# Kernel tuning notes

Measured on AMD Instinct MI355X. Metric: run time of the kernel, lower is better.

The kernel has to match this reference:

```python
import jax, jax.numpy as jnp
import numpy as np

N, E = 50000, 800000
NFEAT, HID, NHEAD, NCLASS = 256, 32, 8, 40
NEG_SLOPE = 0.2


def gat_conv(x, src, dst, W, a_src, a_dst, bias, heads, out_ch, concat):
    n = x.shape[0]
    h = (x @ W).reshape(n, heads, out_ch)              # [N, H, C]
    alpha_src = jnp.einsum('nhc,hc->nh', h, a_src)     # [N, H]
    alpha_dst = jnp.einsum('nhc,hc->nh', h, a_dst)
    e = jax.nn.leaky_relu(alpha_src[src] + alpha_dst[dst], NEG_SLOPE)  # [E, H]
    # segment softmax over incoming edges of each dst node
    m = jax.ops.segment_max(e, dst, num_segments=n)
    ex = jnp.exp(e - m[dst])
    s = jax.ops.segment_sum(ex, dst, num_segments=n)
    alpha = ex / (s[dst] + 1e-16)                      # [E, H]
    out = jax.ops.segment_sum(h[src] * alpha[:, :, None], dst, num_segments=n)  # [N, H, C]
    out = out.reshape(n, heads * out_ch) if concat else out.mean(axis=1)
    return out + bias


def setup_inputs() -> dict:
    key = jax.random.key(0)
    ks = jax.random.split(key, 12)
    x = jax.random.normal(ks[0], (N, NFEAT), dtype=jnp.float32)
    edge_index = jax.random.randint(ks[1], (2, E), 0, N, dtype=jnp.int64)
    edge_attr = jax.random.normal(ks[2], (E, 8), dtype=jnp.float32)  # unused by the model
    s1 = 1.0 / np.sqrt(NFEAT)
    s2 = 1.0 / np.sqrt(HID * NHEAD)
    W1 = jax.random.normal(ks[3], (NFEAT, NHEAD * HID), dtype=jnp.float32) * s1
    att_src1 = jax.random.normal(ks[4], (NHEAD, HID), dtype=jnp.float32) * 0.1
    att_dst1 = jax.random.normal(ks[5], (NHEAD, HID), dtype=jnp.float32) * 0.1
    b1 = jnp.zeros((NHEAD * HID,), dtype=jnp.float32)
    W2 = jax.random.normal(ks[6], (NHEAD * HID, NCLASS), dtype=jnp.float32) * s2
    att_src2 = jax.random.normal(ks[7], (1, NCLASS), dtype=jnp.float32) * 0.1
    att_dst2 = jax.random.normal(ks[8], (1, NCLASS), dtype=jnp.float32) * 0.1
    b2 = jnp.zeros((NCLASS,), dtype=jnp.float32)
    return {"x": x, "edge_index": edge_index, "edge_attr": edge_attr,
            "W1": W1, "att_src1": att_src1, "att_dst1": att_dst1, "b1": b1,
            "W2": W2, "att_src2": att_src2, "att_dst2": att_dst2, "b2": b2}


def reference(x, edge_index, edge_attr, W1, att_src1, att_dst1, b1, W2, att_src2, att_dst2, b2):
    # eval mode: dropout is identity. GATConv adds self-loops by default.
    n = x.shape[0]
    loops = jnp.arange(n, dtype=edge_index.dtype)
    src = jnp.concatenate([edge_index[0], loops])
    dst = jnp.concatenate([edge_index[1], loops])
    h = jax.nn.elu(gat_conv(x, src, dst, W1, att_src1, att_dst1, b1, NHEAD, HID, True))
    final = gat_conv(h, src, dst, W2, att_src2, att_dst2, b2, 1, NCLASS, False)
    return final, jax.nn.log_softmax(final, axis=1)
```

## Files before the change

kernel.cpp:

```cpp
#include <hip/hip_runtime.h>
#include <hip/hip_bf16.h>
#include <hip/hip_fp16.h>
#include <math.h>

#define NN 50000
#define EE 800000
#define ET 850000
#define F1 256
#define NHEAD 8
#define HID 32
#define NCLASS 40
#define NEG 0.2f

typedef __attribute__((ext_vector_type(8))) _Float16 half8_t;
typedef __attribute__((ext_vector_type(4))) float float4_t;

__device__ __forceinline__ int clampN(int v) {
    return v < 0 ? 0 : (v >= NN ? NN - 1 : v);
}
__device__ __forceinline__ unsigned short f2h(float f) {
    __half h = __float2half(f);
    return __builtin_bit_cast(unsigned short, h);
}
__device__ __forceinline__ float h2f(unsigned short u) {
    __half h = __builtin_bit_cast(__half, u);
    return __half2float(h);
}
__device__ __forceinline__ float hlo2f(unsigned int u) {
    return h2f((unsigned short)(u & 0xFFFFu));
}
__device__ __forceinline__ float hhi2f(unsigned int u) {
    return h2f((unsigned short)(u >> 16));
}

__global__ __launch_bounds__(256) void hist_kernel(const int* __restrict__ ei, int* __restrict__ deg,
                                                   unsigned int* __restrict__ pack) {
    int t = blockIdx.x * 256 + threadIdx.x;
    if (t >= ET) return;
    int d = (t < EE) ? ei[EE + t] : (t - EE);
    d = clampN(d);
    int r = atomicAdd(&deg[d], 1);
    pack[t] = ((unsigned)d << 15) | (unsigned)r;
}

__global__ __launch_bounds__(256) void scan1_kernel(const int* __restrict__ deg, int* __restrict__ off, int* __restrict__ bsum) {
    __shared__ int lds[256];
    int b = blockIdx.x, tid = threadIdx.x;
    int base = b * 1024 + tid * 4;
    int v0 = (base + 0 < NN) ? deg[base + 0] : 0;
    int v1 = (base + 1 < NN) ? deg[base + 1] : 0;
    int v2 = (base + 2 < NN) ? deg[base + 2] : 0;
    int v3 = (base + 3 < NN) ? deg[base + 3] : 0;
    int s1 = v0 + v1, s2 = s1 + v2, s3 = s2 + v3;
    lds[tid] = s3;
    __syncthreads();
    for (int o = 1; o < 256; o <<= 1) {
        int t = (tid >= o) ? lds[tid - o] : 0;
        __syncthreads();
        if (tid >= o) lds[tid] += t;
        __syncthreads();
    }
    int excl = tid ? lds[tid - 1] : 0;
    if (base + 0 < NN) off[base + 1] = excl + v0;
    if (base + 1 < NN) off[base + 2] = excl + s1;
    if (base + 2 < NN) off[base + 3] = excl + s2;
    if (base + 3 < NN) off[base + 4] = excl + s3;
    if (tid == 255) bsum[b] = lds[255];
}

__global__ __launch_bounds__(256) void scan2_kernel(int* __restrict__ bsum, int nb) {
    __shared__ int lds[256];
    int tid = threadIdx.x;
    lds[tid] = (tid < nb) ? bsum[tid] : 0;
    __syncthreads();
    for (int o = 1; o < 256; o <<= 1) {
        int t = (tid >= o) ? lds[tid - o] : 0;
        __syncthreads();
        if (tid >= o) lds[tid] += t;
        __syncthreads();
    }
    if (tid < nb) bsum[tid] = lds[tid];
}

__global__ __launch_bounds__(256) void scan3_kernel(int* __restrict__ off, const int* __restrict__ bsum) {
    int b = blockIdx.x, tid = threadIdx.x;
    if (b == 0 && tid == 0) off[0] = 0;
    if (b == 0) return;
    int add = bsum[b - 1];
    int base = b * 1024 + tid * 4;
    #pragma unroll
    for (int i = 0; i < 4; ++i) {
        if (base + i < NN) off[base + i + 1] += add;
    }
}

__global__ __launch_bounds__(256) void scatter_kernel(const int* __restrict__ ei, const int* __restrict__ off,
                                                      const unsigned int* __restrict__ pack, int* __restrict__ esrc) {
    int t = blockIdx.x * 256 + threadIdx.x;
    if (t >= ET) return;
    unsigned p = pack[t];
    int d = p >> 15;
    int r = p & 0x7FFF;
    int s = (t < EE) ? ei[t] : (t - EE);
    s = clampN(s);
    esrc[off[d] + r] = s;
}

__global__ __launch_bounds__(256) void prep_kernel(const float* __restrict__ W1,
                                                   const float* __restrict__ as1, const float* __restrict__ ad1,
                                                   const float* __restrict__ W2,
                                                   const float* __restrict__ ats2, const float* __restrict__ atd2,
                                                   unsigned short* __restrict__ Bt1,
                                                   unsigned short* __restrict__ Bt2) {
    int n = blockIdx.x;
    int k = threadIdx.x;
    if (n < 272) {
        float v;
        if (n < 256) {
            v = W1[(size_t)k * 256 + n];
        } else {
            int j = n - 256;
            int h = j & 7;
            const float* att = (j < 8) ? (as1 + h * 32) : (ad1 + h * 32);
            float s = 0.f;
            #pragma unroll
            for (int c = 0; c < 32; ++c) s += W1[(size_t)k * 256 + h * 32 + c] * att[c];
            v = s;
        }
        Bt1[n * 256 + k] = f2h(v);
    } else {
        int n2 = n - 272;
        float v = 0.f;
        if (n2 < NCLASS) {
            v = W2[(size_t)k * NCLASS + n2];
        } else if (n2 == NCLASS) {
            #pragma unroll
            for (int j = 0; j < NCLASS; ++j) v += W2[(size_t)k * NCLASS + j] * ats2[j];
        } else if (n2 == NCLASS + 1) {
            #pragma unroll
            for (int j = 0; j < NCLASS; ++j) v += W2[(size_t)k * NCLASS + j] * atd2[j];
        }
        Bt2[n2 * 256 + k] = f2h(v);
    }
}

#define AKP 40
__global__ __launch_bounds__(256, 2) void gemm1_kernel(const float* __restrict__ x,
                                                       const unsigned short* __restrict__ Bt,
                                                       unsigned short* __restrict__ h1b,
                                                       float* __restrict__ asrc1, float* __restrict__ adst1) {
    __shared__ __align__(16) unsigned short Ah[128 * AKP];
    __shared__ __align__(16) unsigned short Bs[272 * AKP];
    int tid = threadIdx.x;
    int wave = tid >> 6, lane = tid & 63;
    int quad = lane >> 4, l16 = lane & 15;
    int row0 = blockIdx.x * 128;

    float4_t acc[2][17];
    #pragma unroll
    for (int i = 0; i < 2; ++i)
        #pragma unroll
        for (int j = 0; j < 17; ++j) acc[i][j] = (float4_t){0.f, 0.f, 0.f, 0.f};

    for (int k0 = 0; k0 < 256; k0 += 32) {
        __syncthreads();
        #pragma unroll
        for (int i = 0; i < 4; ++i) {
            int id = i * 256 + tid;
            int r = id >> 3, kq = id & 7;
            int rr = row0 + r; if (rr >= NN) rr = NN - 1;
            float4 v = *(const float4*)(x + (size_t)rr * 256 + k0 + kq * 4);
            ushort4 hi;
            hi.x = f2h(v.x);
            hi.y = f2h(v.y);
            hi.z = f2h(v.z);
            hi.w = f2h(v.w);
            *(ushort4*)(Ah + r * AKP + kq * 4) = hi;
        }
        for (int id = tid; id < 272 * 4; id += 256) {
            int r = id >> 2, kq = id & 3;
            *(float4*)(Bs + r * AKP + kq * 8) = *(const float4*)(Bt + (size_t)r * 256 + k0 + kq * 8);
        }
        __syncthreads();
        half8_t ah[2];
        #pragma unroll
        for (int mt = 0; mt < 2; ++mt) {
            int mrow = wave * 32 + mt * 16 + l16;
            ah[mt] = *(const half8_t*)(Ah + mrow * AKP + quad * 8);
        }
        #pragma unroll
        for (int nt = 0; nt < 17; ++nt) {
            int nrow = nt * 16 + l16;
            half8_t bh = *(const half8_t*)(Bs + nrow * AKP + quad * 8);
            #pragma unroll
            for (int mt = 0; mt < 2; ++mt) {
                acc[mt][nt] = __builtin_amdgcn_mfma_f32_16x16x32_f16(ah[mt], bh, acc[mt][nt], 0, 0, 0);
            }
        }
    }
    #pragma unroll
    for (int mt = 0; mt < 2; ++mt) {
        int rbase = row0 + wave * 32 + mt * 16 + quad * 4;
        #pragma unroll
        for (int r = 0; r < 4; ++r) {
            int row = rbase + r;
            if (row >= NN) continue;
            #pragma unroll
            for (int nt = 0; nt < 16; ++nt)
                h1b[(size_t)row * 256 + nt * 16 + l16] = f2h(acc[mt][nt][r]);
            float v = acc[mt][16][r];
            if (l16 < 8) asrc1[row * 8 + l16] = v;
            else         adst1[row * 8 + (l16 - 8)] = v;
        }
    }
}

#define WST 68
__global__ __launch_bounds__(256) void agg1_kernel(const unsigned short* __restrict__ h1b, const float* __restrict__ asrc,
                                                   const float* __restrict__ adst, const int* __restrict__ esrc,
                                                   const int* __restrict__ off,
                                                   const float* __restrict__ b1, unsigned short* __restrict__ hout) {
    __shared__ __align__(16) float wl[4][8 * WST];
    __shared__ __align__(16) int  snl[4][64];
    int tid = threadIdx.x;
    int wave = tid >> 6;
    int wid = blockIdx.x * 4 + wave;
    if (wid >= NN) return;
    int lane = tid & 63;
    int hp = lane & 7;
    int jp = lane >> 3;
    int hc = lane >> 3;
    int c0 = lane * 4;
    float* wlw = wl[wave];
    int* snw = snl[wave];
    const float* wrow = wlw + hc * WST;
    const char* hb = (const char*)h1b;
    unsigned lofs = (unsigned)c0 * 2;
    float adh_p = adst[wid * 8 + hp];
    int e0 = off[wid], e1 = off[wid + 1];

    float s = 0.f;
    float ax = 0.f, ay = 0.f, az = 0.f, aw = 0.f;

    for (int base = e0; base < e1; base += 64) {
        int cnt = e1 - base; if (cnt > 64) cnt = 64;
        int snv = esrc[base + (lane < cnt ? lane : cnt - 1)];
        snw[lane] = snv;
        int nch = (cnt + 7) >> 3;
        #pragma unroll
        for (int cj = 0; cj < 8; ++cj) {
            if (cj >= nch) break;
            int jedge = cj * 8 + jp;
            int sj = __shfl(snv, jedge);
            float a = asrc[sj * 8 + hp];
            float e = a + adh_p;
            e = (e >= 0.f) ? e : NEG * e;
            float w = (jedge < cnt) ? __expf(e) : 0.f;
            s += w;
            wlw[hp * WST + cj * 8 + jp] = w;
        }
        int nslots = nch * 8;
        for (int j = 0; j < nslots; j += 8) {
            float4 wa = *(const float4*)(wrow + j);
            float4 wb = *(const float4*)(wrow + j + 4);
            int4 sa = *(const int4*)(snw + j);
            int4 sb = *(const int4*)(snw + j + 4);
            const char* r0 = hb + ((size_t)(unsigned)__builtin_amdgcn_readfirstlane(sa.x) << 9);
            const char* r1 = hb + ((size_t)(unsigned)__builtin_amdgcn_readfirstlane(sa.y) << 9);
            const char* r2 = hb + ((size_t)(unsigned)__builtin_amdgcn_readfirstlane(sa.z) << 9);
            const char* r3 = hb + ((size_t)(unsigned)__builtin_amdgcn_readfirstlane(sa.w) << 9);
            const char* r4 = hb + ((size_t)(unsigned)__builtin_amdgcn_readfirstlane(sb.x) << 9);
            const char* r5 = hb + ((size_t)(unsigned)__builtin_amdgcn_readfirstlane(sb.y) << 9);
            const char* r6 = hb + ((size_t)(unsigned)__builtin_amdgcn_readfirstlane(sb.z) << 9);
            const char* r7 = hb + ((size_t)(unsigned)__builtin_amdgcn_readfirstlane(sb.w) << 9);
            uint2 u0 = *(const uint2*)(r0 + lofs);
            uint2 u1 = *(const uint2*)(r1 + lofs);
            uint2 u2 = *(const uint2*)(r2 + lofs);
            uint2 u3 = *(const uint2*)(r3 + lofs);
            uint2 u4 = *(const uint2*)(r4 + lofs);
            uint2 u5 = *(const uint2*)(r5 + lofs);
            uint2 u6 = *(const uint2*)(r6 + lofs);
            uint2 u7 = *(const uint2*)(r7 + lofs);
            ax += wa.x * hlo2f(u0.x);
            ay += wa.x * hhi2f(u0.x);
            az += wa.x * hlo2f(u0.y);
            aw += wa.x * hhi2f(u0.y);
            ax += wa.y * hlo2f(u1.x);
            ay += wa.y * hhi2f(u1.x);
            az += wa.y * hlo2f(u1.y);
            aw += wa.y * hhi2f(u1.y);
            ax += wa.z * hlo2f(u2.x);
            ay += wa.z * hhi2f(u2.x);
            az += wa.z * hlo2f(u2.y);
            aw += wa.z * hhi2f(u2.y);
            ax += wa.w * hlo2f(u3.x);
            ay += wa.w * hhi2f(u3.x);
            az += wa.w * hlo2f(u3.y);
            aw += wa.w * hhi2f(u3.y);
            ax += wb.x * hlo2f(u4.x);
            ay += wb.x * hhi2f(u4.x);
            az += wb.x * hlo2f(u4.y);
            aw += wb.x * hhi2f(u4.y);
            ax += wb.y * hlo2f(u5.x);
            ay += wb.y * hhi2f(u5.x);
            az += wb.y * hlo2f(u5.y);
            aw += wb.y * hhi2f(u5.y);
            ax += wb.z * hlo2f(u6.x);
            ay += wb.z * hhi2f(u6.x);
            az += wb.z * hlo2f(u6.y);
            aw += wb.z * hhi2f(u6.y);
            ax += wb.w * hlo2f(u7.x);
            ay += wb.w * hhi2f(u7.x);
            az += wb.w * hlo2f(u7.y);
            aw += wb.w * hhi2f(u7.y);
        }
    }
    s += __shfl_xor(s, 8);
    s += __shfl_xor(s, 16);
    s += __shfl_xor(s, 32);
    float sh = __shfl(s, hc);
    float inv = 1.f / (sh + 1e-16f);
    float4 b = *(const float4*)(b1 + c0);
    float vx = ax * inv + b.x, vy = ay * inv + b.y, vz = az * inv + b.z, vw = aw * inv + b.w;
    ushort4 o;
    o.x = f2h((vx > 0.f) ? vx : expm1f(vx));
    o.y = f2h((vy > 0.f) ? vy : expm1f(vy));
    o.z = f2h((vz > 0.f) ? vz : expm1f(vz));
    o.w = f2h((vw > 0.f) ? vw : expm1f(vw));
    *(ushort4*)(hout + (size_t)wid * 256 + c0) = o;
}

#define BKP 40
__global__ __launch_bounds__(256, 2) void gemm2_kernel(const unsigned short* __restrict__ h,
                                                       const unsigned short* __restrict__ Bt2,
                                                       unsigned short* __restrict__ h2b, float* __restrict__ as2,
                                                       float* __restrict__ ad2) {
    __shared__ __align__(16) unsigned short Ah[128 * BKP];
    __shared__ __align__(16) unsigned short Bs[48 * BKP];
    int tid = threadIdx.x;
    int wave = tid >> 6, lane = tid & 63;
    int quad = lane >> 4, l16 = lane & 15;
    int row0 = blockIdx.x * 128;

    float4_t acc[2][3];
    #pragma unroll
    for (int i = 0; i < 2; ++i)
        #pragma unroll
        for (int j = 0; j < 3; ++j) acc[i][j] = (float4_t){0.f, 0.f, 0.f, 0.f};

    for (int k0 = 0; k0 < 256; k0 += 32) {
        __syncthreads();
        #pragma unroll
        for (int i = 0; i < 2; ++i) {
            int id = i * 256 + tid;
            int r = id >> 2, kq = id & 3;
            int rr = row0 + r; if (rr >= NN) rr = NN - 1;
            *(float4*)(Ah + r * BKP + kq * 8) = *(const float4*)(h + (size_t)rr * 256 + k0 + kq * 8);
        }
        if (tid < 192) {
            int r = tid >> 2, kq = tid & 3;
            *(float4*)(Bs + r * BKP + kq * 8) = *(const float4*)(Bt2 + (size_t)r * 256 + k0 + kq * 8);
        }
        __syncthreads();
        half8_t ah[2];
        #pragma unroll
        for (int mt = 0; mt < 2; ++mt) {
            int mrow = wave * 32 + mt * 16 + l16;
            ah[mt] = *(const half8_t*)(Ah + mrow * BKP + quad * 8);
        }
        #pragma unroll
        for (int nt = 0; nt < 3; ++nt) {
            int nrow = nt * 16 + l16;
            half8_t bh = *(const half8_t*)(Bs + nrow * BKP + quad * 8);
            #pragma unroll
            for (int mt = 0; mt < 2; ++mt) {
                acc[mt][nt] = __builtin_amdgcn_mfma_f32_16x16x32_f16(ah[mt], bh, acc[mt][nt], 0, 0, 0);
            }
        }
    }
    #pragma unroll
    for (int mt = 0; mt < 2; ++mt) {
        int rbase = row0 + wave * 32 + mt * 16 + quad * 4;
        #pragma unroll
        for (int r = 0; r < 4; ++r) {
            int row = rbase + r;
            if (row >= NN) continue;
            #pragma unroll
            for (int nt = 0; nt < 3; ++nt) {
                int j = nt * 16 + l16;
                float v = acc[mt][nt][r];
                if (j < NCLASS)            h2b[(size_t)row * 40 + j] = f2h(v);
                else if (j == NCLASS)      as2[row] = v;
                else if (j == NCLASS + 1)  ad2[row] = v;
            }
        }
    }
}

__global__ __launch_bounds__(256) void agg2_kernel(const unsigned short* __restrict__ h2b, const float* __restrict__ asrc,
                                                   const float* __restrict__ adst, const int* __restrict__ esrc,
                                                   const int* __restrict__ off,
                                                   const float* __restrict__ b2, float* __restrict__ outF,
                                                   float* __restrict__ outL) {
    __shared__ __align__(16) float wl2[4][64];
    __shared__ __align__(16) int  snl2[4][64];
    int tid = threadIdx.x;
    int wave = tid >> 6;
    int wid = blockIdx.x * 4 + wave;
    if (wid >= NN) return;
    int lane = tid & 63;
    int c = lane;
    const char* hb = (const char*)h2b;
    unsigned coff = (unsigned)(c < NCLASS ? c : 0) * 2;
    float* wlw = wl2[wave];
    int* snw = snl2[wave];
    float bc = (c < NCLASS) ? b2[c] : 0.f;
    float adh = adst[wid];
    int e0 = off[wid], e1 = off[wid + 1];

    float s = 0.f, acc = 0.f;

    for (int base = e0; base < e1; base += 64) {
        int cnt = e1 - base; if (cnt > 64) cnt = 64;
        int snv = esrc[base + (lane < cnt ? lane : cnt - 1)];
        snw[lane] = snv;
        float a = asrc[snv];
        float e = a + adh;
        e = (e >= 0.f) ? e : NEG * e;
        float w = (lane < cnt) ? __expf(e) : 0.f;
        s += w;
        wlw[lane] = w;
        int n16 = (cnt + 15) & ~15;
        for (int j = 0; j < n16; j += 16) {
            float4 wa = *(const float4*)(wlw + j);
            float4 wb = *(const float4*)(wlw + j + 4);
            float4 wc = *(const float4*)(wlw + j + 8);
            float4 wd = *(const float4*)(wlw + j + 12);
            int4 sa = *(const int4*)(snw + j);
            int4 sb = *(const int4*)(snw + j + 4);
            int4 sc = *(const int4*)(snw + j + 8);
            int4 sd = *(const int4*)(snw + j + 12);
            const char* r0 = hb + (size_t)((unsigned)__builtin_amdgcn_readfirstlane(sa.x) * 80u);
            const char* r1 = hb + (size_t)((unsigned)__builtin_amdgcn_readfirstlane(sa.y) * 80u);
            const char* r2 = hb + (size_t)((unsigned)__builtin_amdgcn_readfirstlane(sa.z) * 80u);
            const char* r3 = hb + (size_t)((unsigned)__builtin_amdgcn_readfirstlane(sa.w) * 80u);
            const char* r4 = hb + (size_t)((unsigned)__builtin_amdgcn_readfirstlane(sb.x) * 80u);
            const char* r5 = hb + (size_t)((unsigned)__builtin_amdgcn_readfirstlane(sb.y) * 80u);
            const char* r6 = hb + (size_t)((unsigned)__builtin_amdgcn_readfirstlane(sb.z) * 80u);
            const char* r7 = hb + (size_t)((unsigned)__builtin_amdgcn_readfirstlane(sb.w) * 80u);
            const char* r8 = hb + (size_t)((unsigned)__builtin_amdgcn_readfirstlane(sc.x) * 80u);
            const char* r9 = hb + (size_t)((unsigned)__builtin_amdgcn_readfirstlane(sc.y) * 80u);
            const char* rA = hb + (size_t)((unsigned)__builtin_amdgcn_readfirstlane(sc.z) * 80u);
            const char* rB = hb + (size_t)((unsigned)__builtin_amdgcn_readfirstlane(sc.w) * 80u);
            const char* rC = hb + (size_t)((unsigned)__builtin_amdgcn_readfirstlane(sd.x) * 80u);
            const char* rD = hb + (size_t)((unsigned)__builtin_amdgcn_readfirstlane(sd.y) * 80u);
            const char* rE = hb + (size_t)((unsigned)__builtin_amdgcn_readfirstlane(sd.z) * 80u);
            const char* rF = hb + (size_t)((unsigned)__builtin_amdgcn_readfirstlane(sd.w) * 80u);
            unsigned short v0 = *(const unsigned short*)(r0 + coff);
            unsigned short v1 = *(const unsigned short*)(r1 + coff);
            unsigned short v2 = *(const unsigned short*)(r2 + coff);
            unsigned short v3 = *(const unsigned short*)(r3 + coff);
            unsigned short v4 = *(const unsigned short*)(r4 + coff);
            unsigned short v5 = *(const unsigned short*)(r5 + coff);
            unsigned short v6 = *(const unsigned short*)(r6 + coff);
            unsigned short v7 = *(const unsigned short*)(r7 + coff);
            unsigned short v8 = *(const unsigned short*)(r8 + coff);
            unsigned short v9 = *(const unsigned short*)(r9 + coff);
            unsigned short vA = *(const unsigned short*)(rA + coff);
            unsigned short vB = *(const unsigned short*)(rB + coff);
            unsigned short vC = *(const unsigned short*)(rC + coff);
            unsigned short vD = *(const unsigned short*)(rD + coff);
            unsigned short vE = *(const unsigned short*)(rE + coff);
            unsigned short vF = *(const unsigned short*)(rF + coff);
            acc += wa.x * h2f(v0);
            acc += wa.y * h2f(v1);
            acc += wa.z * h2f(v2);
            acc += wa.w * h2f(v3);
            acc += wb.x * h2f(v4);
            acc += wb.y * h2f(v5);
            acc += wb.z * h2f(v6);
            acc += wb.w * h2f(v7);
            acc += wc.x * h2f(v8);
            acc += wc.y * h2f(v9);
            acc += wc.z * h2f(vA);
            acc += wc.w * h2f(vB);
            acc += wd.x * h2f(vC);
            acc += wd.y * h2f(vD);
            acc += wd.z * h2f(vE);
            acc += wd.w * h2f(vF);
        }
    }
    s += __shfl_xor(s, 1);
    s += __shfl_xor(s, 2);
    s += __shfl_xor(s, 4);
    s += __shfl_xor(s, 8);
    s += __shfl_xor(s, 16);
    s += __shfl_xor(s, 32);
    float inv = 1.f / (s + 1e-16f);
    float fin = (c < NCLASS) ? (acc * inv + bc) : -INFINITY;
    if (c < NCLASS) outF[(size_t)wid * 40 + c] = fin;
    float mx = fin;
    for (int o = 32; o; o >>= 1) mx = fmaxf(mx, __shfl_xor(mx, o));
    float ex = (c < NCLASS) ? __expf(fin - mx) : 0.f;
    float sm = ex;
    for (int o = 32; o; o >>= 1) sm += __shfl_xor(sm, o);
    if (c < NCLASS) outL[(size_t)wid * 40 + c] = fin - mx - __logf(sm);
}

extern "C" void kernel_launch(void* const* d_in, const int* in_sizes, int n_in,
                              void* d_out, int out_size, void* d_ws, size_t ws_size,
                              hipStream_t stream) {
    const float* x   = (const float*)d_in[0];
    const int*   ei  = (const int*)d_in[1];
    const float* W1  = (const float*)d_in[3];
    const float* as1 = (const float*)d_in[4];
    const float* ad1 = (const float*)d_in[5];
    const float* b1  = (const float*)d_in[6];
    const float* W2  = (const float*)d_in[7];
    const float* as2c = (const float*)d_in[8];
    const float* ad2c = (const float*)d_in[9];
    const float* b2  = (const float*)d_in[10];

    float* outF = (float*)d_out;
    float* outL = outF + (size_t)NN * NCLASS;

    char* w = (char*)d_ws;
    auto alloc = [&](size_t bytes) {
        void* p = (void*)w;
        w += (bytes + 255) & ~(size_t)255;
        return p;
    };
    unsigned short* h1b = (unsigned short*)alloc((size_t)NN * 256 * 2);
    unsigned short* hbuf = (unsigned short*)alloc((size_t)NN * 256 * 2);
    unsigned short* h2b = (unsigned short*)alloc((size_t)NN * 40 * 2);
    float* asrc1 = (float*)alloc((size_t)NN * 8 * 4);
    float* adst1 = (float*)alloc((size_t)NN * 8 * 4);
    float* asrc2 = (float*)alloc((size_t)NN * 4);
    float* adst2 = (float*)alloc((size_t)NN * 4);
    int* deg    = (int*)alloc((size_t)NN * 4);
    int* off    = (int*)alloc((size_t)(NN + 1) * 4);
    unsigned int* pack = (unsigned int*)alloc((size_t)ET * 4);
    int* esrc   = (int*)alloc((size_t)ET * 4);
    int* bsum   = (int*)alloc(64 * 4);
    unsigned short* W1th = (unsigned short*)alloc((size_t)272 * 256 * 2);
    unsigned short* W2t  = (unsigned short*)alloc((size_t)48 * 256 * 2);

    const int NB_SCAN = (NN + 1023) / 1024;

    hipMemsetAsync(deg, 0, (size_t)NN * 4, stream);

    hist_kernel<<<(ET + 255) / 256, 256, 0, stream>>>(ei, deg, pack);
    scan1_kernel<<<NB_SCAN, 256, 0, stream>>>(deg, off, bsum);
    scan2_kernel<<<1, 256, 0, stream>>>(bsum, NB_SCAN);
    scan3_kernel<<<NB_SCAN, 256, 0, stream>>>(off, bsum);
    scatter_kernel<<<(ET + 255) / 256, 256, 0, stream>>>(ei, off, pack, esrc);

    prep_kernel<<<320, 256, 0, stream>>>(W1, as1, ad1, W2, as2c, ad2c, W1th, W2t);
    gemm1_kernel<<<(NN + 127) / 128, 256, 0, stream>>>(x, W1th, h1b, asrc1, adst1);
    agg1_kernel<<<(NN + 3) / 4, 256, 0, stream>>>(h1b, asrc1, adst1, esrc, off, b1, hbuf);
    gemm2_kernel<<<(NN + 127) / 128, 256, 0, stream>>>(hbuf, W2t, h2b, asrc2, adst2);
    agg2_kernel<<<(NN + 3) / 4, 256, 0, stream>>>(h2b, asrc2, adst2, esrc, off, b2, outF, outL);
}
```

Before: 314.3 us.

## Merge independent graph-build and weight-prep kernels into shared launches

Packs the weight transpose/prep blocks together with the degree histogram blocks in one launch, and packs the CSR scatter blocks together with the first GEMM blocks in another. The goal is to cut two kernel launches and let independent work overlap on the GPU instead of running serially. The cost is that the scatter blocks carry the GEMM kernel's large LDS allocation and launch bounds, which may lower their occupancy. Block scheduling order may also delay GEMM tiles behind the scatter blocks.

```diff
diff --git a/kernel.cpp b/kernel.cpp
--- a/kernel.cpp
+++ b/kernel.cpp
@@ -12,6 +12,10 @@
 #define NCLASS 40
 #define NEG 0.2f
 
+#define NB_HIST ((ET + 255) / 256)
+#define NB_PREP 320
+#define NB_G1   ((NN + 127) / 128)
+
 typedef __attribute__((ext_vector_type(8))) _Float16 half8_t;
 typedef __attribute__((ext_vector_type(4))) float float4_t;
 
@@ -33,14 +37,54 @@
     return h2f((unsigned short)(u >> 16));
 }
 
-__global__ __launch_bounds__(256) void hist_kernel(const int* __restrict__ ei, int* __restrict__ deg,
-                                                   unsigned int* __restrict__ pack) {
-    int t = blockIdx.x * 256 + threadIdx.x;
-    if (t >= ET) return;
-    int d = (t < EE) ? ei[EE + t] : (t - EE);
-    d = clampN(d);
-    int r = atomicAdd(&deg[d], 1);
-    pack[t] = ((unsigned)d << 15) | (unsigned)r;
+__global__ __launch_bounds__(256) void fusedA_kernel(const int* __restrict__ ei, int* __restrict__ deg,
+                                                     unsigned int* __restrict__ pack,
+                                                     const float* __restrict__ W1,
+                                                     const float* __restrict__ as1, const float* __restrict__ ad1,
+                                                     const float* __restrict__ W2,
+                                                     const float* __restrict__ ats2, const float* __restrict__ atd2,
+                                                     unsigned short* __restrict__ Bt1,
+                                                     unsigned short* __restrict__ Bt2) {
+    int blk = blockIdx.x;
+    if (blk < NB_PREP) {
+        int n = blk;
+        int k = threadIdx.x;
+        if (n < 272) {
+            float v;
+            if (n < 256) {
+                v = W1[(size_t)k * 256 + n];
+            } else {
+                int j = n - 256;
+                int h = j & 7;
+                const float* att = (j < 8) ? (as1 + h * 32) : (ad1 + h * 32);
+                float s = 0.f;
+                #pragma unroll
+                for (int c = 0; c < 32; ++c) s += W1[(size_t)k * 256 + h * 32 + c] * att[c];
+                v = s;
+            }
+            Bt1[n * 256 + k] = f2h(v);
+        } else {
+            int n2 = n - 272;
+            float v = 0.f;
+            if (n2 < NCLASS) {
+                v = W2[(size_t)k * NCLASS + n2];
+            } else if (n2 == NCLASS) {
+                #pragma unroll
+                for (int j = 0; j < NCLASS; ++j) v += W2[(size_t)k * NCLASS + j] * ats2[j];
+            } else if (n2 == NCLASS + 1) {
+                #pragma unroll
+                for (int j = 0; j < NCLASS; ++j) v += W2[(size_t)k * NCLASS + j] * atd2[j];
+            }
+            Bt2[n2 * 256 + k] = f2h(v);
+        }
+    } else {
+        int t = (blk - NB_PREP) * 256 + threadIdx.x;
+        if (t >= ET) return;
+        int d = (t < EE) ? ei[EE + t] : (t - EE);
+        d = clampN(d);
+        int r = atomicAdd(&deg[d], 1);
+        pack[t] = ((unsigned)d << 15) | (unsigned)r;
+    }
 }
 
 __global__ __launch_bounds__(256) void scan1_kernel(const int* __restrict__ deg, int* __restrict__ off, int* __restrict__ bsum) {
@@ -94,63 +138,26 @@
     }
 }
 
-__global__ __launch_bounds__(256) void scatter_kernel(const int* __restrict__ ei, const int* __restrict__ off,
-                                                      const unsigned int* __restrict__ pack, int* __restrict__ esrc) {
-    int t = blockIdx.x * 256 + threadIdx.x;
-    if (t >= ET) return;
-    unsigned p = pack[t];
-    int d = p >> 15;
-    int r = p & 0x7FFF;
-    int s = (t < EE) ? ei[t] : (t - EE);
-    s = clampN(s);
-    esrc[off[d] + r] = s;
-}
-
-__global__ __launch_bounds__(256) void prep_kernel(const float* __restrict__ W1,
-                                                   const float* __restrict__ as1, const float* __restrict__ ad1,
-                                                   const float* __restrict__ W2,
-                                                   const float* __restrict__ ats2, const float* __restrict__ atd2,
-                                                   unsigned short* __restrict__ Bt1,
-                                                   unsigned short* __restrict__ Bt2) {
-    int n = blockIdx.x;
-    int k = threadIdx.x;
-    if (n < 272) {
-        float v;
-        if (n < 256) {
-            v = W1[(size_t)k * 256 + n];
-        } else {
-            int j = n - 256;
-            int h = j & 7;
-            const float* att = (j < 8) ? (as1 + h * 32) : (ad1 + h * 32);
-            float s = 0.f;
-            #pragma unroll
-            for (int c = 0; c < 32; ++c) s += W1[(size_t)k * 256 + h * 32 + c] * att[c];
-            v = s;
-        }
-        Bt1[n * 256 + k] = f2h(v);
-    } else {
-        int n2 = n - 272;
-        float v = 0.f;
-        if (n2 < NCLASS) {
-            v = W2[(size_t)k * NCLASS + n2];
-        } else if (n2 == NCLASS) {
-            #pragma unroll
-            for (int j = 0; j < NCLASS; ++j) v += W2[(size_t)k * NCLASS + j] * ats2[j];
-        } else if (n2 == NCLASS + 1) {
-            #pragma unroll
-            for (int j = 0; j < NCLASS; ++j) v += W2[(size_t)k * NCLASS + j] * atd2[j];
-        }
-        Bt2[n2 * 256 + k] = f2h(v);
-    }
-}
-
 #define AKP 40
-__global__ __launch_bounds__(256, 2) void gemm1_kernel(const float* __restrict__ x,
-                                                       const unsigned short* __restrict__ Bt,
-                                                       unsigned short* __restrict__ h1b,
-                                                       float* __restrict__ asrc1, float* __restrict__ adst1) {
+__global__ __launch_bounds__(256, 2) void fusedB_kernel(const float* __restrict__ x,
+                                                        const unsigned short* __restrict__ Bt,
+                                                        unsigned short* __restrict__ h1b,
+                                                        float* __restrict__ asrc1, float* __restrict__ adst1,
+                                                        const int* __restrict__ ei, const int* __restrict__ off,
+                                                        const unsigned int* __restrict__ pack, int* __restrict__ esrc) {
     __shared__ __align__(16) unsigned short Ah[128 * AKP];
     __shared__ __align__(16) unsigned short Bs[272 * AKP];
+    if (blockIdx.x >= NB_G1) {
+        int t = (blockIdx.x - NB_G1) * 256 + threadIdx.x;
+        if (t >= ET) return;
+        unsigned p = pack[t];
+        int d = p >> 15;
+        int r = p & 0x7FFF;
+        int s = (t < EE) ? ei[t] : (t - EE);
+        s = clampN(s);
+        esrc[off[d] + r] = s;
+        return;
+    }
     int tid = threadIdx.x;
     int wave = tid >> 6, lane = tid & 63;
     int quad = lane >> 4, l16 = lane & 15;
@@ -549,14 +556,11 @@
 
     hipMemsetAsync(deg, 0, (size_t)NN * 4, stream);
 
-    hist_kernel<<<(ET + 255) / 256, 256, 0, stream>>>(ei, deg, pack);
+    fusedA_kernel<<<NB_PREP + NB_HIST, 256, 0, stream>>>(ei, deg, pack, W1, as1, ad1, W2, as2c, ad2c, W1th, W2t);
     scan1_kernel<<<NB_SCAN, 256, 0, stream>>>(deg, off, bsum);
     scan2_kernel<<<1, 256, 0, stream>>>(bsum, NB_SCAN);
     scan3_kernel<<<NB_SCAN, 256, 0, stream>>>(off, bsum);
-    scatter_kernel<<<(ET + 255) / 256, 256, 0, stream>>>(ei, off, pack, esrc);
-
-    prep_kernel<<<320, 256, 0, stream>>>(W1, as1, ad1, W2, as2c, ad2c, W1th, W2t);
-    gemm1_kernel<<<(NN + 127) / 128, 256, 0, stream>>>(x, W1th, h1b, asrc1, adst1);
+    fusedB_kernel<<<NB_G1 + NB_HIST, 256, 0, stream>>>(x, W1th, h1b, asrc1, adst1, ei, off, pack, esrc);
     agg1_kernel<<<(NN + 3) / 4, 256, 0, stream>>>(h1b, asrc1, adst1, esrc, off, b1, hbuf);
     gemm2_kernel<<<(NN + 127) / 128, 256, 0, stream>>>(hbuf, W2t, h2b, asrc2, adst2);
     agg2_kernel<<<(NN + 3) / 4, 256, 0, stream>>>(h2b, asrc2, adst2, esrc, off, b2, outF, outL);
```

Measured after the change: 308.4 us. About the same (-1.9%).
